# Optimization experiments

Hardware: AMD Instinct MI355X
Metric: run time of the kernel (lower is better)

## Reference

```python
import jax, jax.numpy as jnp
import numpy as np

B, Q, WAY, SHOT, H, W, C = 2, 75, 5, 5, 10, 10, 640
NEIGHBOR_K = 5


def setup_inputs() -> dict:
    key = jax.random.key(0)
    k1, k2 = jax.random.split(key)
    input1 = jax.random.normal(k1, (B, Q, H, W, C), dtype=jnp.float32)
    # per the original unpacking: dim1=shot, dim2=way
    input2 = jax.random.normal(k2, (B, SHOT, WAY, H, W, C), dtype=jnp.float32)
    return {"input1": input1, "input2": input2, "neighbor_k": NEIGHBOR_K}


def reference(input1, input2, neighbor_k):
    # input1: [b, q_num, h, w, c] query local descriptors
    # input2: [b, shot, way, h, w, c] support local descriptors
    b, q_num, h, w, c = input1.shape
    _, shot, way, _, _, _ = input2.shape
    hw = h * w

    q = input1.reshape(b, q_num, hw, c)
    s = input2.reshape(b, way * shot, hw, c)

    # L2-normalize each local descriptor over channel dim
    q = q / jnp.linalg.norm(q, axis=-1, keepdims=True)
    s = s / jnp.linalg.norm(s, axis=-1, keepdims=True)

    # group support descriptors per class: [b, way, shot*hw, c]
    # (matches torch .view semantics on the contiguous flattened buffer)
    support = s.reshape(b, way, shot * hw, c)

    # cosine similarity between every query patch and every support patch
    # scores: [b, q_num, way, hw, shot*hw]
    scores = jnp.einsum('bqpc,bwsc->bqwps', q, support)

    # top-k nearest support descriptors per query patch, mean over k
    topv, _ = jax.lax.top_k(scores, neighbor_k)          # [b,q,way,hw,k]
    sim_local = jnp.sum(topv, axis=-1) / neighbor_k      # [b,q,way,hw]
    sim_way = jnp.sum(sim_local, axis=-1)                # [b,q,way]
    return sim_way
```

## Files before the change

kernel.cpp:

```cpp
#include <hip/hip_runtime.h>

#define QN    75
#define HWN   100
#define CN    640
#define NSUP  500
#define MROWS 7500
#define NQD   (2 * MROWS)
#define NSD   5000
#define NDESC (NQD + NSD)
#define MT    128
#define NT    256
#define BK    64
#define CST   272

typedef __attribute__((ext_vector_type(8))) __bf16 bf16x8;
typedef __attribute__((ext_vector_type(4))) float  f32x4;

#define GLDS(gp, lp) __builtin_amdgcn_global_load_lds(                        \
    (const __attribute__((address_space(1))) void*)(gp),                      \
    (__attribute__((address_space(3))) void*)(lp), 16, 0, 0)

static __device__ inline unsigned short f2bf(float f) {
    unsigned int u = __float_as_uint(f);
    u += 0x7fffu + ((u >> 16) & 1u);
    return (unsigned short)(u >> 16);
}

__global__ __launch_bounds__(256) void prep_kernel(const float* __restrict__ q,
                                                   const float* __restrict__ s,
                                                   unsigned short* __restrict__ qbf,
                                                   unsigned short* __restrict__ sbf) {
    int wave = (blockIdx.x * 256 + threadIdx.x) >> 6;
    int lane = threadIdx.x & 63;
    if (wave >= NDESC) return;
    const float* src = (wave < NQD) ? (q + (size_t)wave * CN)
                                    : (s + (size_t)(wave - NQD) * CN);
    unsigned short* dst = (wave < NQD) ? (qbf + (size_t)wave * CN)
                                       : (sbf + (size_t)(wave - NQD) * CN);
    float4 v[3];
    float ss = 0.f;
#pragma unroll
    for (int j = 0; j < 3; ++j) {
        int idx4 = lane + 64 * j;
        if (idx4 < CN / 4) {
            v[j] = *(const float4*)(src + idx4 * 4);
            ss = fmaf(v[j].x, v[j].x, ss);
            ss = fmaf(v[j].y, v[j].y, ss);
            ss = fmaf(v[j].z, v[j].z, ss);
            ss = fmaf(v[j].w, v[j].w, ss);
        }
    }
#pragma unroll
    for (int off = 32; off > 0; off >>= 1)
        ss += __shfl_xor(ss, off, 64);
    float inv = rsqrtf(ss);
#pragma unroll
    for (int j = 0; j < 3; ++j) {
        int idx4 = lane + 64 * j;
        if (idx4 < CN / 4) {
            ushort4 o;
            o.x = f2bf(v[j].x * inv);
            o.y = f2bf(v[j].y * inv);
            o.z = f2bf(v[j].z * inv);
            o.w = f2bf(v[j].w * inv);
            *(ushort4*)(dst + idx4 * 4) = o;
        }
    }
}

__global__ __launch_bounds__(512, 4) void mfma_kernel(const unsigned short* __restrict__ qbf,
                                                      const unsigned short* __restrict__ sbf,
                                                      float* __restrict__ part) {
    const int xcd = blockIdx.x & 7;
    const int idx = blockIdx.x >> 3;
    const int b   = xcd >> 2;
    const int mbq = xcd & 3;
    const int mbsz = (mbq < 3) ? 15 : 14;
    if (idx >= 10 * mbsz) return;
    const int g  = idx / (2 * mbsz);
    const int r_ = idx % (2 * mbsz);
    const int nc = r_ / mbsz;
    const int mb = mbq * 15 + (r_ % mbsz);
    const int bg = b * 5 + g;
    const int r0 = mb * MT;
    const int c0 = nc * NT;

    __shared__ __align__(16) char smem[49152];
    unsigned short* Alds = (unsigned short*)smem;
    unsigned short* Blds = (unsigned short*)(smem + 16384);
    float*          Cst  = (float*)smem;

    const int t    = threadIdx.x;
    const int lane = t & 63;
    const int wid  = t >> 6;
    const int h    = wid >> 2;
    const int colq = wid & 3;

    const unsigned short* qptr = qbf + (size_t)b * MROWS * CN;
    const unsigned short* sptr = sbf + (size_t)(b * 25 + g * 5) * HWN * CN;

    f32x4 acc[4][4];
#pragma unroll
    for (int mt = 0; mt < 4; ++mt)
#pragma unroll
        for (int nt = 0; nt < 4; ++nt)
            acc[mt][nt] = (f32x4)0.f;

    const int lx   = lane >> 3;
    const int ls   = lane & 7;
    const int gsrc = ls ^ lx;

    int ar0 = r0 + wid * 16 + lx;       if (ar0 > MROWS - 1) ar0 = MROWS - 1;
    int ar1 = r0 + wid * 16 + 8 + lx;   if (ar1 > MROWS - 1) ar1 = MROWS - 1;
    const int aoff0 = ar0 * CN + gsrc * 8;
    const int aoff1 = ar1 * CN + gsrc * 8;
    char* aldst = smem + wid * 2048;

    int boff[4];
#pragma unroll
    for (int c = 0; c < 4; ++c) {
        int col = c0 + wid * 32 + c * 8 + lx;
        if (col > NSUP - 1) col = NSUP - 1;
        boff[c] = col * CN + gsrc * 8;
    }
    char* bldst = smem + 16384 + wid * 4096;

    const int q_ = lane >> 4;
    const int lr = lane & 15;
    const int sw = lr & 7;

    for (int k0 = 0; k0 < CN; k0 += BK) {
        __syncthreads();
        GLDS(qptr + aoff0 + k0, aldst);
        GLDS(qptr + aoff1 + k0, aldst + 1024);
#pragma unroll
        for (int c = 0; c < 4; ++c)
            GLDS(sptr + boff[c] + k0, bldst + c * 1024);
        __syncthreads();

#pragma unroll
        for (int ks = 0; ks < 2; ++ks) {
            const int sl = ((ks * 4 + q_) ^ sw) * 8;
            bf16x8 af[4];
#pragma unroll
            for (int mt = 0; mt < 4; ++mt)
                af[mt] = *(const bf16x8*)(Alds + (h * 64 + mt * 16 + lr) * 64 + sl);
#pragma unroll
            for (int nt = 0; nt < 4; ++nt) {
                bf16x8 bfr = *(const bf16x8*)(Blds + (colq * 64 + nt * 16 + lr) * 64 + sl);
#pragma unroll
                for (int mt = 0; mt < 4; ++mt)
                    acc[mt][nt] = __builtin_amdgcn_mfma_f32_16x16x32_bf16(af[mt], bfr, acc[mt][nt], 0, 0, 0);
            }
        }
    }

    const int erow = t >> 4;
    const int es   = t & 15;
#define CE(a, b) { float hi_ = fmaxf(a, b), lo_ = fminf(a, b); a = hi_; b = lo_; }
#pragma unroll
    for (int mt = 0; mt < 4; ++mt) {
        __syncthreads();
#pragma unroll
        for (int nt = 0; nt < 4; ++nt)
#pragma unroll
            for (int e = 0; e < 4; ++e)
                Cst[(h * 16 + q_ * 4 + e) * CST + colq * 64 + nt * 16 + lr] = acc[mt][nt][e];
        __syncthreads();

        float t0 = -3.4e38f, t1 = -3.4e38f, t2 = -3.4e38f, t3 = -3.4e38f, t4 = -3.4e38f;
#pragma unroll
        for (int i = 0; i < 16; ++i) {
            int col = es + 16 * i;
            float v = (c0 + col < NSUP) ? Cst[erow * CST + col] : -3.4e38f;
            float hi;
            hi = fmaxf(t0, v); v = fminf(t0, v); t0 = hi;
            hi = fmaxf(t1, v); v = fminf(t1, v); t1 = hi;
            hi = fmaxf(t2, v); v = fminf(t2, v); t2 = hi;
            hi = fmaxf(t3, v); v = fminf(t3, v); t3 = hi;
            hi = fmaxf(t4, v); v = fminf(t4, v); t4 = hi;
        }
#pragma unroll
        for (int d = 1; d < 16; d <<= 1) {
            float b0 = __shfl_xor(t0, d, 64);
            float b1 = __shfl_xor(t1, d, 64);
            float b2 = __shfl_xor(t2, d, 64);
            float b3 = __shfl_xor(t3, d, 64);
            float b4 = __shfl_xor(t4, d, 64);
            t0 = fmaxf(t0, b4); t1 = fmaxf(t1, b3); t2 = fmaxf(t2, b2);
            t3 = fmaxf(t3, b1); t4 = fmaxf(t4, b0);
            CE(t0, t1); CE(t2, t3);
            CE(t1, t2); CE(t3, t4);
            CE(t0, t1); CE(t2, t3);
            CE(t1, t2); CE(t3, t4);
            CE(t0, t1); CE(t2, t3);
        }
        if (es == 0) {
            int patch = r0 + (erow >> 4) * 64 + mt * 16 + (erow & 15);
            if (patch < MROWS) {
                float* pp = part + ((size_t)(bg * MROWS + patch) * 2 + nc) * 5;
                pp[0] = t0; pp[1] = t1; pp[2] = t2; pp[3] = t3; pp[4] = t4;
            }
        }
    }
#undef CE
}

__global__ __launch_bounds__(256) void merge_kernel(const float* __restrict__ part,
                                                    float* __restrict__ out) {
    int w    = (blockIdx.x * 256 + threadIdx.x) >> 6;
    int lane = threadIdx.x & 63;
    if (w >= 750) return;
    int b  = w / 375, r = w % 375;
    int qi = r / 5,   g = r % 5;
    int bg = b * 5 + g;

    float sum = 0.f;
    for (int p = lane; p < HWN; p += 64) {
        int row = qi * HWN + p;
        const float* pp = part + (size_t)(bg * MROWS + row) * 10;
        float t0 = -3.4e38f, t1 = -3.4e38f, t2 = -3.4e38f, t3 = -3.4e38f, t4 = -3.4e38f;
#pragma unroll
        for (int j = 0; j < 10; ++j) {
            float v = pp[j], hi;
            hi = fmaxf(t0, v); v = fminf(t0, v); t0 = hi;
            hi = fmaxf(t1, v); v = fminf(t1, v); t1 = hi;
            hi = fmaxf(t2, v); v = fminf(t2, v); t2 = hi;
            hi = fmaxf(t3, v); v = fminf(t3, v); t3 = hi;
            hi = fmaxf(t4, v); v = fminf(t4, v); t4 = hi;
        }
        sum += (t0 + t1 + t2 + t3 + t4) * 0.2f;
    }
#pragma unroll
    for (int off = 32; off > 0; off >>= 1)
        sum += __shfl_xor(sum, off, 64);
    if (lane == 0) out[w] = sum;
}

extern "C" void kernel_launch(void* const* d_in, const int* in_sizes, int n_in,
                              void* d_out, int out_size, void* d_ws, size_t ws_size,
                              hipStream_t stream) {
    const float* in1 = (const float*)d_in[0];
    const float* in2 = (const float*)d_in[1];
    float* out = (float*)d_out;

    unsigned short* qbf  = (unsigned short*)d_ws;
    unsigned short* sbf  = qbf + (size_t)NQD * CN;
    float*          part = (float*)(sbf + (size_t)NSD * CN);

    prep_kernel<<<dim3(NDESC / 4), 256, 0, stream>>>(in1, in2, qbf, sbf);
    mfma_kernel<<<dim3(1200), 512, 0, stream>>>(qbf, sbf, part);
    merge_kernel<<<dim3(188), 256, 0, stream>>>(part, out);
}
```

Before: 160.2 us.

## Double-buffer LDS tiles with BK=32 to overlap global loads with MFMA

Halves the K-step to 32 and splits shared memory into two 24KB buffers so the next K-slice is loaded with global_load_lds while MFMAs run on the current one. This removes one barrier per iteration and lets memory latency overlap with compute. The swizzle pattern and load mapping are reworked for the 32-wide rows. The cost is twice as many loop iterations with less work each, and there is no explicit vmcnt wait before the barrier, so correctness depends on __syncthreads draining the async LDS loads.

```diff
diff --git a/kernel.cpp b/kernel.cpp
--- a/kernel.cpp
+++ b/kernel.cpp
@@ -10,7 +10,7 @@
 #define NDESC (NQD + NSD)
 #define MT    128
 #define NT    256
-#define BK    64
+#define BK    32
 #define CST   272
 
 typedef __attribute__((ext_vector_type(8))) __bf16 bf16x8;
@@ -86,9 +86,7 @@
     const int c0 = nc * NT;
 
     __shared__ __align__(16) char smem[49152];
-    unsigned short* Alds = (unsigned short*)smem;
-    unsigned short* Blds = (unsigned short*)(smem + 16384);
-    float*          Cst  = (float*)smem;
+    float* Cst = (float*)smem;
 
     const int t    = threadIdx.x;
     const int lane = t & 63;
@@ -106,53 +104,54 @@
         for (int nt = 0; nt < 4; ++nt)
             acc[mt][nt] = (f32x4)0.f;
 
-    const int lx   = lane >> 3;
-    const int ls   = lane & 7;
-    const int gsrc = ls ^ lx;
-
-    int ar0 = r0 + wid * 16 + lx;       if (ar0 > MROWS - 1) ar0 = MROWS - 1;
-    int ar1 = r0 + wid * 16 + 8 + lx;   if (ar1 > MROWS - 1) ar1 = MROWS - 1;
-    const int aoff0 = ar0 * CN + gsrc * 8;
-    const int aoff1 = ar1 * CN + gsrc * 8;
-    char* aldst = smem + wid * 2048;
-
-    int boff[4];
-#pragma unroll
-    for (int c = 0; c < 4; ++c) {
-        int col = c0 + wid * 32 + c * 8 + lx;
+    const int lsub = lane >> 2;
+    const int gsrc = (lane & 3) ^ ((lane >> 3) & 3);
+
+    int arow = r0 + wid * 16 + lsub; if (arow > MROWS - 1) arow = MROWS - 1;
+    const int aoff = arow * CN + gsrc * 8;
+    const int adst = wid * 1024;
+
+    int boff[2];
+#pragma unroll
+    for (int j = 0; j < 2; ++j) {
+        int col = c0 + j * 128 + wid * 16 + lsub;
         if (col > NSUP - 1) col = NSUP - 1;
-        boff[c] = col * CN + gsrc * 8;
-    }
-    char* bldst = smem + 16384 + wid * 4096;
+        boff[j] = col * CN + gsrc * 8;
+    }
+    const int bdst0 = 8192 + wid * 1024;
 
     const int q_ = lane >> 4;
     const int lr = lane & 15;
-    const int sw = lr & 7;
-
+    const int sl = (q_ ^ ((lr >> 1) & 3)) * 8;
+
+    GLDS(qptr + aoff, smem + adst);
+    GLDS(sptr + boff[0], smem + bdst0);
+    GLDS(sptr + boff[1], smem + bdst0 + 8192);
+    __syncthreads();
+
+    int p = 0;
     for (int k0 = 0; k0 < CN; k0 += BK) {
+        if (k0 + BK < CN) {
+            char* nb = smem + (p ^ 1) * 24576;
+            GLDS(qptr + aoff + k0 + BK, nb + adst);
+            GLDS(sptr + boff[0] + k0 + BK, nb + bdst0);
+            GLDS(sptr + boff[1] + k0 + BK, nb + bdst0 + 8192);
+        }
+        const unsigned short* Alds = (const unsigned short*)(smem + p * 24576);
+        const unsigned short* Blds = Alds + 4096;
+        bf16x8 af[4];
+#pragma unroll
+        for (int mt = 0; mt < 4; ++mt)
+            af[mt] = *(const bf16x8*)(Alds + (h * 64 + mt * 16 + lr) * 32 + sl);
+#pragma unroll
+        for (int nt = 0; nt < 4; ++nt) {
+            bf16x8 bfr = *(const bf16x8*)(Blds + (colq * 64 + nt * 16 + lr) * 32 + sl);
+#pragma unroll
+            for (int mt = 0; mt < 4; ++mt)
+                acc[mt][nt] = __builtin_amdgcn_mfma_f32_16x16x32_bf16(af[mt], bfr, acc[mt][nt], 0, 0, 0);
+        }
         __syncthreads();
-        GLDS(qptr + aoff0 + k0, aldst);
-        GLDS(qptr + aoff1 + k0, aldst + 1024);
-#pragma unroll
-        for (int c = 0; c < 4; ++c)
-            GLDS(sptr + boff[c] + k0, bldst + c * 1024);
-        __syncthreads();
-
-#pragma unroll
-        for (int ks = 0; ks < 2; ++ks) {
-            const int sl = ((ks * 4 + q_) ^ sw) * 8;
-            bf16x8 af[4];
-#pragma unroll
-            for (int mt = 0; mt < 4; ++mt)
-                af[mt] = *(const bf16x8*)(Alds + (h * 64 + mt * 16 + lr) * 64 + sl);
-#pragma unroll
-            for (int nt = 0; nt < 4; ++nt) {
-                bf16x8 bfr = *(const bf16x8*)(Blds + (colq * 64 + nt * 16 + lr) * 64 + sl);
-#pragma unroll
-                for (int mt = 0; mt < 4; ++mt)
-                    acc[mt][nt] = __builtin_amdgcn_mfma_f32_16x16x32_bf16(af[mt], bfr, acc[mt][nt], 0, 0, 0);
-            }
-        }
+        p ^= 1;
     }
 
     const int erow = t >> 4;
```

Result: slower. 164.1 us (+2.4%).

## Fuse top-k merge into MFMA kernel via last-arriver atomic counter

Applied to the files above, without the earlier changes.

Removes the separate merge kernel. The second of the two column-half blocks for each row tile merges both partial top-5 lists and atomically adds the per-patch mean into the output. Each block signals arrival on a per-tile counter after a threadfence. This saves a kernel launch and the extra pass, at the cost of two memsets, float atomics on the output (order-dependent rounding), and some tail work in the GEMM kernel.

```diff
diff --git a/kernel.cpp b/kernel.cpp
--- a/kernel.cpp
+++ b/kernel.cpp
@@ -70,7 +70,9 @@
 
 __global__ __launch_bounds__(512, 4) void mfma_kernel(const unsigned short* __restrict__ qbf,
                                                       const unsigned short* __restrict__ sbf,
-                                                      float* __restrict__ part) {
+                                                      float* __restrict__ part,
+                                                      int* __restrict__ ready,
+                                                      float* __restrict__ out) {
     const int xcd = blockIdx.x & 7;
     const int idx = blockIdx.x >> 3;
     const int b   = xcd >> 2;
@@ -86,6 +88,7 @@
     const int c0 = nc * NT;
 
     __shared__ __align__(16) char smem[49152];
+    __shared__ int winner;
     unsigned short* Alds = (unsigned short*)smem;
     unsigned short* Blds = (unsigned short*)(smem + 16384);
     float*          Cst  = (float*)smem;
@@ -204,37 +207,31 @@
         }
     }
 #undef CE
-}
-
-__global__ __launch_bounds__(256) void merge_kernel(const float* __restrict__ part,
-                                                    float* __restrict__ out) {
-    int w    = (blockIdx.x * 256 + threadIdx.x) >> 6;
-    int lane = threadIdx.x & 63;
-    if (w >= 750) return;
-    int b  = w / 375, r = w % 375;
-    int qi = r / 5,   g = r % 5;
-    int bg = b * 5 + g;
-
-    float sum = 0.f;
-    for (int p = lane; p < HWN; p += 64) {
-        int row = qi * HWN + p;
-        const float* pp = part + (size_t)(bg * MROWS + row) * 10;
-        float t0 = -3.4e38f, t1 = -3.4e38f, t2 = -3.4e38f, t3 = -3.4e38f, t4 = -3.4e38f;
-#pragma unroll
-        for (int j = 0; j < 10; ++j) {
-            float v = pp[j], hi;
-            hi = fmaxf(t0, v); v = fminf(t0, v); t0 = hi;
-            hi = fmaxf(t1, v); v = fminf(t1, v); t1 = hi;
-            hi = fmaxf(t2, v); v = fminf(t2, v); t2 = hi;
-            hi = fmaxf(t3, v); v = fminf(t3, v); t3 = hi;
-            hi = fmaxf(t4, v); v = fminf(t4, v); t4 = hi;
-        }
-        sum += (t0 + t1 + t2 + t3 + t4) * 0.2f;
-    }
-#pragma unroll
-    for (int off = 32; off > 0; off >>= 1)
-        sum += __shfl_xor(sum, off, 64);
-    if (lane == 0) out[w] = sum;
+
+    __threadfence();
+    if (t == 0) {
+        int old = atomicAdd(&ready[bg * 59 + mb], 1);
+        winner = (old == 1);
+    }
+    __syncthreads();
+    if (winner && t < MT) {
+        int row = r0 + t;
+        if (row < MROWS) {
+            const float* pp = part + (size_t)(bg * MROWS + row) * 10;
+            float t0 = -3.4e38f, t1 = -3.4e38f, t2 = -3.4e38f, t3 = -3.4e38f, t4 = -3.4e38f;
+#pragma unroll
+            for (int j = 0; j < 10; ++j) {
+                float v = pp[j], hi;
+                hi = fmaxf(t0, v); v = fminf(t0, v); t0 = hi;
+                hi = fmaxf(t1, v); v = fminf(t1, v); t1 = hi;
+                hi = fmaxf(t2, v); v = fminf(t2, v); t2 = hi;
+                hi = fmaxf(t3, v); v = fminf(t3, v); t3 = hi;
+                hi = fmaxf(t4, v); v = fminf(t4, v); t4 = hi;
+            }
+            atomicAdd(&out[(b * QN + row / HWN) * 5 + g],
+                      (t0 + t1 + t2 + t3 + t4) * 0.2f);
+        }
+    }
 }
 
 extern "C" void kernel_launch(void* const* d_in, const int* in_sizes, int n_in,
@@ -247,8 +244,11 @@
     unsigned short* qbf  = (unsigned short*)d_ws;
     unsigned short* sbf  = qbf + (size_t)NQD * CN;
     float*          part = (float*)(sbf + (size_t)NSD * CN);
+    int*            ready = (int*)(part + 750000);
+
+    hipMemsetAsync(d_out, 0, (size_t)out_size * sizeof(float), stream);
+    hipMemsetAsync(ready, 0, 590 * sizeof(int), stream);
 
     prep_kernel<<<dim3(NDESC / 4), 256, 0, stream>>>(in1, in2, qbf, sbf);
-    mfma_kernel<<<dim3(1200), 512, 0, stream>>>(qbf, sbf, part);
-    merge_kernel<<<dim3(188), 256, 0, stream>>>(part, out);
-}
+    mfma_kernel<<<dim3(1200), 512, 0, stream>>>(qbf, sbf, part, ready, out);
+}
```

Result: slower. 358.4 us (+123.7%).
